# Kernel tuning notes

Measured on AMD Instinct MI355X. Metric: run time of the kernel, lower is better.

Reference implementation:

```python
import jax, jax.numpy as jnp
import numpy as np
import math

EMBED_DIM = 256
NUM_HEADS = 8
FFN_DIM = 1024
EPS = 1e-5


def layer_norm(x, g, b):
    mu = jnp.mean(x, axis=-1, keepdims=True)
    var = jnp.var(x, axis=-1, keepdims=True)
    return (x - mu) / jnp.sqrt(var + EPS) * g + b


def setup_inputs() -> dict:
    key = jax.random.key(0)
    ks = jax.random.split(key, 10)
    B, L, D, F = 4, 2048, EMBED_DIM, FFN_DIM
    x = jax.random.normal(ks[0], (B, L, D), dtype=jnp.float32)
    mask = jnp.ones((B, L), dtype=jnp.int32)
    # FFN params (PyTorch Linear default-ish scale)
    W1 = jax.random.normal(ks[1], (D, F), dtype=jnp.float32) / np.sqrt(D)
    b1 = jnp.zeros((F,), dtype=jnp.float32)
    W2 = jax.random.normal(ks[2], (F, D), dtype=jnp.float32) / np.sqrt(F)
    b2 = jnp.zeros((D,), dtype=jnp.float32)
    g1 = jnp.ones((D,), dtype=jnp.float32)
    be1 = jnp.zeros((D,), dtype=jnp.float32)
    g2 = jnp.ones((D,), dtype=jnp.float32)
    be2 = jnp.zeros((D,), dtype=jnp.float32)
    return {"x": x, "mask": mask, "W1": W1, "b1": b1, "W2": W2, "b2": b2,
            "g1": g1, "be1": be1, "g2": g2, "be2": be2}


def quantum_attention(x, mask):
    B, L, D = x.shape
    H, dk = NUM_HEADS, D // NUM_HEADS
    xh = x.reshape(B, L, H, dk).transpose(0, 2, 1, 3)  # [B,H,L,dk]
    # per-token mean over batch and heads -> [L, dk]
    m = jnp.mean(xh, axis=(0, 1))
    # closed form of the single-qubit RX circuit: P(|1>) = sin^2(angle/2)
    dot = m @ m.T  # [L, L]
    ang = jnp.clip(dot, -math.pi, math.pi)
    scores = jnp.sin(ang * 0.5) ** 2  # [L, L], shared across B and H
    attn = jnp.broadcast_to(scores[None, None], (B, H, L, L))
    attn = jnp.where(mask[:, None, None, :] == 0, -1e9, attn)
    attn = jax.nn.softmax(attn, axis=-1)
    out = jnp.einsum('bhij,bhjd->bhid', attn, xh)  # values are xh itself
    return out.transpose(0, 2, 1, 3).reshape(B, L, D)


def reference(x, mask, W1, b1, W2, b2, g1, be1, g2, be2):
    attn_out = quantum_attention(x, mask)
    h = layer_norm(x + attn_out, g1, be1)
    ffn = jax.nn.relu(h @ W1 + b1) @ W2 + b2
    return layer_norm(h + ffn, g2, be2)
```

## Files before the change

### kernel.cpp

```cpp
#include <hip/hip_runtime.h>
#include <hip/hip_bf16.h>


#define B_ 4
#define L_ 2048
#define D_ 256
#define F_ 1024
#define PI_F 3.14159265358979323846f

typedef __bf16 bf16x8 __attribute__((ext_vector_type(8)));
typedef float floatx4 __attribute__((ext_vector_type(4)));
typedef unsigned short ushortx4 __attribute__((ext_vector_type(4)));

#define WAIT_VM(n) asm volatile("s_waitcnt vmcnt(" #n ")" ::: "memory")
#define SCHED0() __builtin_amdgcn_sched_barrier(0)
#define BARRIER() do { SCHED0(); __builtin_amdgcn_s_barrier(); SCHED0(); } while (0)

__device__ __forceinline__ unsigned short f2bf(float f) {
    unsigned int u = __float_as_uint(f);
    u = (u + 0x7FFFu + ((u >> 16) & 1u)) >> 16;
    return (unsigned short)u;
}
__device__ __forceinline__ float bf2f(unsigned short u) {
    union { unsigned int i; float f; } v; v.i = ((unsigned int)u) << 16; return v.f;
}

__device__ __forceinline__ void async_cp16(unsigned short* lds, const unsigned short* g) {
    __builtin_amdgcn_global_load_lds(
        (const __attribute__((address_space(1))) unsigned int*)g,
        (__attribute__((address_space(3))) unsigned int*)lds, 16, 0, 0);
}

__global__ __launch_bounds__(256) void k_prep(const float* __restrict__ x,
                                              const float* __restrict__ W1,
                                              const float* __restrict__ W2,
                                              const int* __restrict__ mask,
                                              unsigned short* __restrict__ mb,
                                              unsigned short* __restrict__ XmT,
                                              unsigned short* __restrict__ W1T,
                                              unsigned short* __restrict__ W2T) {
    __shared__ float tile[32][33];
    int r = blockIdx.x, t = threadIdx.x;
    if (r >= 2560) {
        if (r < 2816) {
            int idx = (r - 2560) * 256 + t;
            int l = idx >> 5, k = idx & 31;
            float s = 0.f;
#pragma unroll
            for (int b = 0; b < B_; b++) {
                const float* xp = x + ((size_t)(b * L_ + l)) * D_ + k;
#pragma unroll
                for (int h = 0; h < 8; h++) s += xp[h * 32];
            }
            mb[idx] = f2bf(s * (1.f / 32.f));
        } else {
#pragma unroll
            for (int c = 0; c < 32; c++) {
                int e = c * 256 + t;
                int b = e >> 11, j = e & (L_ - 1);
                XmT[(size_t)(1024 + b) * L_ + j] = mask[b * L_ + j] ? 0x3F80 : 0;
            }
        }
        return;
    }
    const float* in; unsigned short* outp; int R, C; const int* mrow = nullptr; size_t bo = 0;
    int bx, by;
    if (r < 2048) {
        int z = r >> 9, rem = r & 511; by = rem >> 3; bx = rem & 7;
        in = x; outp = XmT; R = L_; C = 256; bo = (size_t)z * R * C; mrow = mask + z * L_;
    } else if (r < 2304) {
        int rem = r - 2048; bx = rem & 31; by = rem >> 5;
        in = W1; outp = W1T; R = 256; C = 1024;
    } else {
        int rem = r - 2304; bx = rem & 7; by = rem >> 3;
        in = W2; outp = W2T; R = 1024; C = 256;
    }
    int r0 = by * 32, c0 = bx * 32;
    int tx = t & 31, ty = t >> 5;
#pragma unroll
    for (int rr = 0; rr < 4; rr++) {
        int rw = ty + rr * 8;
        tile[rw][tx] = in[bo + (size_t)(r0 + rw) * C + c0 + tx];
    }
    float mfac = 1.f;
    if (mrow) mfac = mrow[r0 + tx] ? 1.f : 0.f;
    __syncthreads();
#pragma unroll
    for (int rr = 0; rr < 4; rr++) {
        int c = ty + rr * 8;
        outp[bo + (size_t)(c0 + c) * R + r0 + tx] = f2bf(tile[tx][c] * mfac);
    }
}

__global__ __launch_bounds__(256) void k_scores_mfma(const unsigned short* __restrict__ mb,
                                                     unsigned short* __restrict__ E) {
    const int t = threadIdx.x, lane = t & 63, wid = t >> 6;
    const int wm = (wid >> 1) * 64, wn = (wid & 1) * 32;
    const int lr = lane & 15, lq = lane >> 4;
    int m0 = blockIdx.y * 128, n0 = blockIdx.x * 64;
    bf16x8 af[4], bfr[2];
#pragma unroll
    for (int i = 0; i < 4; i++)
        af[i] = *(const bf16x8*)(mb + (size_t)(m0 + wm + i * 16 + lr) * 32 + lq * 8);
#pragma unroll
    for (int j = 0; j < 2; j++)
        bfr[j] = *(const bf16x8*)(mb + (size_t)(n0 + wn + j * 16 + lr) * 32 + lq * 8);
    floatx4 acc[4][2];
#pragma unroll
    for (int i = 0; i < 4; i++)
#pragma unroll
        for (int j = 0; j < 2; j++) {
            acc[i][j] = (floatx4){0.f, 0.f, 0.f, 0.f};
            acc[i][j] = __builtin_amdgcn_mfma_f32_16x16x32_bf16(af[i], bfr[j], acc[i][j], 0, 0, 0);
        }
#pragma unroll
    for (int i = 0; i < 4; i++)
#pragma unroll
        for (int j = 0; j < 2; j++)
#pragma unroll
            for (int r = 0; r < 4; r++) {
                int row = m0 + wm + i * 16 + lq * 4 + r;
                int col = n0 + wn + j * 16 + lr;
                float d = fminf(fmaxf(acc[i][j][r], -PI_F), PI_F);
                float sn = __sinf(0.5f * d);
                E[(size_t)row * L_ + col] = f2bf(__expf(sn * sn));
            }
}

__global__ __launch_bounds__(256) void k_av(const unsigned short* __restrict__ E,
                                            const unsigned short* __restrict__ XmT,
                                            unsigned short* __restrict__ Cb) {
    __shared__ __align__(16) unsigned short sbuf[3][128 * 64 + 64 * 64];
    const int t = threadIdx.x, lane = t & 63, wid = t >> 6;
    const int wm = (wid >> 1) * 64, wn = (wid & 1) * 32;
    const int lr = lane & 15, lq = lane >> 4;
    const int lrow = lane >> 3, lseg = lane & 7;

    int bid = blockIdx.x;
    int swz = (bid & 7) * 34 + (bid >> 3);
    int m0 = (swz / 17) * 128, n0 = (swz % 17) * 64;

    const unsigned short* Ag[4]; int sAoff[4];
#pragma unroll
    for (int q = 0; q < 4; q++) {
        int rl = wid * 32 + q * 8 + lrow;
        Ag[q] = E + (size_t)(m0 + rl) * L_ + ((lseg - rl) & 7) * 8;
        sAoff[q] = (wid * 32 + q * 8) * 64;
    }
    const unsigned short* Bg[2]; int sBoff[2];
#pragma unroll
    for (int q = 0; q < 2; q++) {
        int rl = wid * 16 + q * 8 + lrow;
        Bg[q] = XmT + (size_t)(n0 + rl) * L_ + ((lseg - rl) & 7) * 8;
        sBoff[q] = 8192 + (wid * 16 + q * 8) * 64;
    }
    int arot[4], aroff[4], brot[2], broff[2];
#pragma unroll
    for (int i = 0; i < 4; i++) { int ar = wm + i * 16 + lr; aroff[i] = ar * 64; arot[i] = lq + ar; }
#pragma unroll
    for (int j = 0; j < 2; j++) { int br = wn + j * 16 + lr; broff[j] = 8192 + br * 64; brot[j] = lq + br; }

    floatx4 acc[4][2];
#pragma unroll
    for (int i = 0; i < 4; i++)
#pragma unroll
        for (int j = 0; j < 2; j++) acc[i][j] = (floatx4){0.f, 0.f, 0.f, 0.f};

    auto stage = [&](unsigned short* base, int k0) {
#pragma unroll
        for (int q = 0; q < 4; q++) async_cp16(base + sAoff[q], Ag[q] + k0);
#pragma unroll
        for (int q = 0; q < 2; q++) async_cp16(base + sBoff[q], Bg[q] + k0);
    };
    auto compute = [&](const unsigned short* base) {
#pragma unroll
        for (int s = 0; s < 2; s++) {
            bf16x8 af[4], bfr[2];
#pragma unroll
            for (int i = 0; i < 4; i++)
                af[i] = *(const bf16x8*)(base + aroff[i] + ((s * 4 + arot[i]) & 7) * 8);
#pragma unroll
            for (int j = 0; j < 2; j++)
                bfr[j] = *(const bf16x8*)(base + broff[j] + ((s * 4 + brot[j]) & 7) * 8);
#pragma unroll
            for (int i = 0; i < 4; i++)
#pragma unroll
                for (int j = 0; j < 2; j++)
                    acc[i][j] = __builtin_amdgcn_mfma_f32_16x16x32_bf16(af[i], bfr[j], acc[i][j], 0, 0, 0);
        }
    };

    unsigned short *p0 = sbuf[0], *p1 = sbuf[1], *p2 = sbuf[2];
    stage(p0, 0); stage(p1, 64); stage(p2, 128);
    WAIT_VM(12); BARRIER();
    for (int p = 0; p < 29; ++p) {
        compute(p0);
        BARRIER();
        stage(p0, (p + 3) << 6);
        WAIT_VM(12); BARRIER();
        unsigned short* tmp = p0; p0 = p1; p1 = p2; p2 = tmp;
    }
    compute(p0);
    BARRIER();
    WAIT_VM(6); BARRIER();
    compute(p1);
    BARRIER();
    WAIT_VM(0); BARRIER();
    compute(p2);

#pragma unroll
    for (int i = 0; i < 4; i++)
#pragma unroll
        for (int j = 0; j < 2; j++)
#pragma unroll
            for (int r = 0; r < 4; r++) {
                int row = m0 + wm + i * 16 + lq * 4 + r;
                int col = n0 + wn + j * 16 + lr;
                Cb[(size_t)row * 1088 + col] = f2bf(acc[i][j][r]);
            }
}

__global__ __launch_bounds__(256) void k_ln1(const float* __restrict__ x, const unsigned short* __restrict__ Cb,
                                             const float* __restrict__ g_, const float* __restrict__ be_,
                                             unsigned short* __restrict__ hb) {
    int t = threadIdx.x, wid = t >> 6, lane = t & 63;
    int tok = (blockIdx.x << 2) + wid;
    int b = tok >> 11, i = tok & (L_ - 1);
    float rs = bf2f(Cb[(size_t)i * 1088 + 1024 + b]);
    float4 xv = *(const float4*)(x + (size_t)tok * D_ + lane * 4);
    ushortx4 cv = *(const ushortx4*)(Cb + (size_t)i * 1088 + b * 256 + lane * 4);
    float v0 = xv.x + bf2f(cv.x) / rs;
    float v1 = xv.y + bf2f(cv.y) / rs;
    float v2 = xv.z + bf2f(cv.z) / rs;
    float v3 = xv.w + bf2f(cv.w) / rs;
    float s  = v0 + v1 + v2 + v3;
    float s2 = v0 * v0 + v1 * v1 + v2 * v2 + v3 * v3;
#pragma unroll
    for (int o = 1; o < 64; o <<= 1) { s += __shfl_xor(s, o); s2 += __shfl_xor(s2, o); }
    float mu = s * (1.f / 256.f);
    float var = s2 * (1.f / 256.f) - mu * mu;
    float r = rsqrtf(var + 1e-5f);
    float4 gv = *(const float4*)(g_ + lane * 4);
    float4 bv = *(const float4*)(be_ + lane * 4);
    ushortx4 o4;
    o4.x = f2bf((v0 - mu) * r * gv.x + bv.x);
    o4.y = f2bf((v1 - mu) * r * gv.y + bv.y);
    o4.z = f2bf((v2 - mu) * r * gv.z + bv.z);
    o4.w = f2bf((v3 - mu) * r * gv.w + bv.w);
    *(ushortx4*)(hb + (size_t)tok * D_ + lane * 4) = o4;
}

__global__ __launch_bounds__(256) void k_gemm1(const unsigned short* __restrict__ hb,
                                               const unsigned short* __restrict__ W1T,
                                               const float* __restrict__ b1, unsigned short* __restrict__ t1) {
    __shared__ __align__(16) unsigned short sbuf[2][128 * 64 + 128 * 64];
    const int t = threadIdx.x, lane = t & 63, wid = t >> 6;
    const int wm = (wid >> 1) * 64, wn = (wid & 1) * 64;
    const int lr = lane & 15, lq = lane >> 4;
    const int lrow8 = lane >> 3, lseg = lane & 7;

    int bid = blockIdx.x;
    int swz = (bid & 7) * 64 + (bid >> 3);
    int m0 = (swz >> 3) * 128, n0 = (swz & 7) * 128;

    const unsigned short* Ag[4]; const unsigned short* Bg[4]; int aoff[4], boff4[4];
#pragma unroll
    for (int q = 0; q < 4; q++) {
        int rl = q * 32 + wid * 8 + lrow8;
        int seg = (lseg - rl) & 7;
        Ag[q] = hb + (size_t)(m0 + rl) * 256 + seg * 8;
        Bg[q] = W1T + (size_t)(n0 + rl) * 256 + seg * 8;
        aoff[q] = (q * 32 + wid * 8) * 64;
        boff4[q] = 8192 + (q * 32 + wid * 8) * 64;
    }
    int arot[4], aroff[4], brot[4], broff[4];
#pragma unroll
    for (int i = 0; i < 4; i++) { int ar = wm + i * 16 + lr; aroff[i] = ar * 64; arot[i] = lq + ar; }
#pragma unroll
    for (int j = 0; j < 4; j++) { int br = wn + j * 16 + lr; broff[j] = 8192 + br * 64; brot[j] = lq + br; }

    floatx4 acc[4][4];
#pragma unroll
    for (int i = 0; i < 4; i++)
#pragma unroll
        for (int j = 0; j < 4; j++) acc[i][j] = (floatx4){0.f, 0.f, 0.f, 0.f};

    auto stage = [&](unsigned short* base, int k0) {
#pragma unroll
        for (int q = 0; q < 4; q++) { async_cp16(base + aoff[q], Ag[q] + k0); async_cp16(base + boff4[q], Bg[q] + k0); }
    };
    auto compute = [&](const unsigned short* base) {
#pragma unroll
        for (int s = 0; s < 2; s++) {
            bf16x8 af[4], bfr[4];
#pragma unroll
            for (int i = 0; i < 4; i++) af[i] = *(const bf16x8*)(base + aroff[i] + ((s * 4 + arot[i]) & 7) * 8);
#pragma unroll
            for (int j = 0; j < 4; j++) bfr[j] = *(const bf16x8*)(base + broff[j] + ((s * 4 + brot[j]) & 7) * 8);
#pragma unroll
            for (int i = 0; i < 4; i++)
#pragma unroll
                for (int j = 0; j < 4; j++)
                    acc[i][j] = __builtin_amdgcn_mfma_f32_16x16x32_bf16(af[i], bfr[j], acc[i][j], 0, 0, 0);
        }
    };

    unsigned short *pa = sbuf[0], *pb = sbuf[1];
    stage(pa, 0); stage(pb, 64);
    WAIT_VM(8); BARRIER();
    compute(pa);
    BARRIER();
    stage(pa, 128);
    WAIT_VM(8); BARRIER();
    compute(pb);
    BARRIER();
    stage(pb, 192);
    WAIT_VM(8); BARRIER();
    compute(pa);
    BARRIER();
    WAIT_VM(0); BARRIER();
    compute(pb);

    float bb[4];
#pragma unroll
    for (int j = 0; j < 4; j++) bb[j] = b1[n0 + wn + j * 16 + lr];
#pragma unroll
    for (int i = 0; i < 4; i++)
#pragma unroll
        for (int j = 0; j < 4; j++) {
            int col = n0 + wn + j * 16 + lr;
#pragma unroll
            for (int r = 0; r < 4; r++) {
                int row = m0 + wm + i * 16 + lq * 4 + r;
                t1[(size_t)row * 1024 + col] = f2bf(fmaxf(acc[i][j][r] + bb[j], 0.f));
            }
        }
}

__global__ __launch_bounds__(256) void k_gemm2ln(const unsigned short* __restrict__ t1,
                                                 const unsigned short* __restrict__ W2T,
                                                 const float* __restrict__ b2,
                                                 const unsigned short* __restrict__ hb,
                                                 const float* __restrict__ g_, const float* __restrict__ be_,
                                                 float* __restrict__ out) {
    __shared__ __align__(16) unsigned short sbuf[3][32 * 64 + 256 * 64];
    __shared__ float red[2][32][2];
    const int t = threadIdx.x, lane = t & 63, wid = t >> 6;
    const int wm = (wid >> 1) * 16, wn = (wid & 1) * 128;
    const int lr = lane & 15, lq = lane >> 4;
    const int lrow8 = lane >> 3, lseg = lane & 7;
    int m0 = blockIdx.x * 32;

    int arl = wid * 8 + lrow8;
    const unsigned short* Ag = t1 + (size_t)(m0 + arl) * 1024 + (((lseg - arl) & 7) * 8);
    int sAoff = (wid * 8) * 64;
    const unsigned short* Bg[8]; int sBoff[8];
#pragma unroll
    for (int q = 0; q < 8; q++) {
        int rl = q * 32 + wid * 8 + lrow8;
        Bg[q] = W2T + (size_t)rl * 1024 + (((lseg - rl) & 7) * 8);
        sBoff[q] = 2048 + (q * 32 + wid * 8) * 64;
    }
    int aroff = (wm + lr) * 64, arot = lq + wm + lr;
    int brot[8], broff[8];
#pragma unroll
    for (int j = 0; j < 8; j++) { int br = wn + j * 16 + lr; broff[j] = 2048 + br * 64; brot[j] = lq + br; }

    floatx4 acc[8];
#pragma unroll
    for (int j = 0; j < 8; j++) acc[j] = (floatx4){0.f, 0.f, 0.f, 0.f};

    auto stage = [&](unsigned short* base, int k0) {
        async_cp16(base + sAoff, Ag + k0);
#pragma unroll
        for (int q = 0; q < 8; q++) async_cp16(base + sBoff[q], Bg[q] + k0);
    };
    auto compute = [&](const unsigned short* base) {
#pragma unroll
        for (int s = 0; s < 2; s++) {
            bf16x8 af = *(const bf16x8*)(base + aroff + ((s * 4 + arot) & 7) * 8);
#pragma unroll
            for (int j = 0; j < 8; j++) {
                bf16x8 bfr = *(const bf16x8*)(base + broff[j] + ((s * 4 + brot[j]) & 7) * 8);
                acc[j] = __builtin_amdgcn_mfma_f32_16x16x32_bf16(af, bfr, acc[j], 0, 0, 0);
            }
        }
    };

    unsigned short *p0 = sbuf[0], *p1 = sbuf[1], *p2 = sbuf[2];
    stage(p0, 0); stage(p1, 64); stage(p2, 128);
    WAIT_VM(18); BARRIER();
    for (int p = 0; p < 13; ++p) {
        compute(p0);
        BARRIER();
        stage(p0, (p + 3) << 6);
        WAIT_VM(18); BARRIER();
        unsigned short* tmp = p0; p0 = p1; p1 = p2; p2 = tmp;
    }
    compute(p0);
    BARRIER();
    WAIT_VM(9); BARRIER();
    compute(p1);
    BARRIER();
    WAIT_VM(0); BARRIER();
    compute(p2);

    float psum[4], psq[4];
#pragma unroll
    for (int r = 0; r < 4; r++) { psum[r] = 0.f; psq[r] = 0.f; }
#pragma unroll
    for (int j = 0; j < 8; j++) {
        int col = wn + j * 16 + lr;
        float bv = b2[col];
#pragma unroll
        for (int r = 0; r < 4; r++) {
            int row = m0 + wm + lq * 4 + r;
            float v = acc[j][r] + bv + bf2f(hb[(size_t)row * 256 + col]);
            acc[j][r] = v;
            psum[r] += v; psq[r] += v * v;
        }
    }
#pragma unroll
    for (int o = 1; o < 16; o <<= 1) {
#pragma unroll
        for (int r = 0; r < 4; r++) { psum[r] += __shfl_xor(psum[r], o); psq[r] += __shfl_xor(psq[r], o); }
    }
    if (lr == 0) {
#pragma unroll
        for (int r = 0; r < 4; r++) {
            int lrow = wm + lq * 4 + r;
            red[wid & 1][lrow][0] = psum[r];
            red[wid & 1][lrow][1] = psq[r];
        }
    }
    __syncthreads();
#pragma unroll
    for (int r = 0; r < 4; r++) {
        int lrow = wm + lq * 4 + r;
        float s = red[0][lrow][0] + red[1][lrow][0];
        float s2 = red[0][lrow][1] + red[1][lrow][1];
        float mu = s * (1.f / 256.f);
        float var = s2 * (1.f / 256.f) - mu * mu;
        float rc = rsqrtf(var + 1e-5f);
        int row = m0 + lrow;
#pragma unroll
        for (int j = 0; j < 8; j++) {
            int col = wn + j * 16 + lr;
            out[(size_t)row * 256 + col] = (acc[j][r] - mu) * rc * g_[col] + be_[col];
        }
    }
}

extern "C" void kernel_launch(void* const* d_in, const int* in_sizes, int n_in,
                              void* d_out, int out_size, void* d_ws, size_t ws_size,
                              hipStream_t stream) {
    const float* x   = (const float*)d_in[0];
    const int*  mask = (const int*)d_in[1];
    const float* W1  = (const float*)d_in[2];
    const float* b1  = (const float*)d_in[3];
    const float* W2  = (const float*)d_in[4];
    const float* b2  = (const float*)d_in[5];
    const float* g1  = (const float*)d_in[6];
    const float* be1 = (const float*)d_in[7];
    const float* g2  = (const float*)d_in[8];
    const float* be2 = (const float*)d_in[9];
    float* out = (float*)d_out;

    char* w = (char*)d_ws;
    unsigned short* mb_   = (unsigned short*)w;  w += 65536 * 2;
    unsigned short* E_    = (unsigned short*)w;  w += (size_t)L_ * L_ * 2;
    unsigned short* XmT_  = (unsigned short*)w;  w += (size_t)1088 * L_ * 2;
    unsigned short* W1T_  = (unsigned short*)w;  w += 262144 * 2;
    unsigned short* W2T_  = (unsigned short*)w;  w += 262144 * 2;
    unsigned short* Cb_   = (unsigned short*)w;  w += (size_t)L_ * 1088 * 2;
    unsigned short* hb_   = (unsigned short*)w;  w += (size_t)8192 * 256 * 2;
    unsigned short* t1_   = (unsigned short*)w;  w += (size_t)8192 * 1024 * 2;

    k_prep<<<2817, 256, 0, stream>>>(x, W1, W2, mask, mb_, XmT_, W1T_, W2T_);
    k_scores_mfma<<<dim3(32, 16), 256, 0, stream>>>(mb_, E_);
    k_av<<<272, 256, 0, stream>>>(E_, XmT_, Cb_);
    k_ln1<<<2048, 256, 0, stream>>>(x, Cb_, g1, be1, hb_);
    k_gemm1<<<512, 256, 0, stream>>>(hb_, W1T_, b1, t1_);
    k_gemm2ln<<<256, 256, 0, stream>>>(t1_, W2T_, b2, hb_, g2, be2, out);
}
```

Measured before the change: 139.9 us.

## Compute softmax row sums in scores kernel and retile gemm2ln warps

The masked softmax denominators were previously produced by extra mask columns in the AV GEMM (1088 wide). They are now computed as per-block partial row sums inside the scores kernel and reduced in the LN1 kernel. This shrinks the AV GEMM to 1024 columns (256 blocks instead of 272), which removes a partial wave and drops the mask-column setup in prep. The gemm2ln kernel is also retiled so each warp covers 32x64 instead of 16x128, sharing B fragments across two A rows, at the cost of a 4-way LDS reduction.

```diff
diff --git a/kernel.cpp b/kernel.cpp
--- a/kernel.cpp
+++ b/kernel.cpp
@@ -42,25 +42,16 @@
     __shared__ float tile[32][33];
     int r = blockIdx.x, t = threadIdx.x;
     if (r >= 2560) {
-        if (r < 2816) {
-            int idx = (r - 2560) * 256 + t;
-            int l = idx >> 5, k = idx & 31;
-            float s = 0.f;
-#pragma unroll
-            for (int b = 0; b < B_; b++) {
-                const float* xp = x + ((size_t)(b * L_ + l)) * D_ + k;
-#pragma unroll
-                for (int h = 0; h < 8; h++) s += xp[h * 32];
-            }
-            mb[idx] = f2bf(s * (1.f / 32.f));
-        } else {
-#pragma unroll
-            for (int c = 0; c < 32; c++) {
-                int e = c * 256 + t;
-                int b = e >> 11, j = e & (L_ - 1);
-                XmT[(size_t)(1024 + b) * L_ + j] = mask[b * L_ + j] ? 0x3F80 : 0;
-            }
-        }
+        int idx = (r - 2560) * 256 + t;
+        int l = idx >> 5, k = idx & 31;
+        float s = 0.f;
+#pragma unroll
+        for (int b = 0; b < B_; b++) {
+            const float* xp = x + ((size_t)(b * L_ + l)) * D_ + k;
+#pragma unroll
+            for (int h = 0; h < 8; h++) s += xp[h * 32];
+        }
+        mb[idx] = f2bf(s * (1.f / 32.f));
         return;
     }
     const float* in; unsigned short* outp; int R, C; const int* mrow = nullptr; size_t bo = 0;
@@ -93,7 +84,10 @@
 }
 
 __global__ __launch_bounds__(256) void k_scores_mfma(const unsigned short* __restrict__ mb,
-                                                     unsigned short* __restrict__ E) {
+                                                     const int* __restrict__ mask,
+                                                     unsigned short* __restrict__ E,
+                                                     float* __restrict__ rowpart) {
+    __shared__ float part[128][2][4];
     const int t = threadIdx.x, lane = t & 63, wid = t >> 6;
     const int wm = (wid >> 1) * 64, wn = (wid & 1) * 32;
     const int lr = lane & 15, lq = lane >> 4;
@@ -113,8 +107,14 @@
             acc[i][j] = (floatx4){0.f, 0.f, 0.f, 0.f};
             acc[i][j] = __builtin_amdgcn_mfma_f32_16x16x32_bf16(af[i], bfr[j], acc[i][j], 0, 0, 0);
         }
-#pragma unroll
-    for (int i = 0; i < 4; i++)
+    float mv[4][2];
+#pragma unroll
+    for (int b = 0; b < 4; b++) {
+        mv[b][0] = mask[b * L_ + n0 + wn + lr] ? 1.f : 0.f;
+        mv[b][1] = mask[b * L_ + n0 + wn + 16 + lr] ? 1.f : 0.f;
+    }
+#pragma unroll
+    for (int i = 0; i < 4; i++) {
 #pragma unroll
         for (int j = 0; j < 2; j++)
 #pragma unroll
@@ -123,8 +123,34 @@
                 int col = n0 + wn + j * 16 + lr;
                 float d = fminf(fmaxf(acc[i][j][r], -PI_F), PI_F);
                 float sn = __sinf(0.5f * d);
-                E[(size_t)row * L_ + col] = f2bf(__expf(sn * sn));
-            }
+                float e = __expf(sn * sn);
+                acc[i][j][r] = e;
+                E[(size_t)row * L_ + col] = f2bf(e);
+            }
+#pragma unroll
+        for (int r = 0; r < 4; r++) {
+            float pb[4];
+#pragma unroll
+            for (int b = 0; b < 4; b++)
+                pb[b] = acc[i][0][r] * mv[b][0] + acc[i][1][r] * mv[b][1];
+#pragma unroll
+            for (int o = 1; o < 16; o <<= 1)
+#pragma unroll
+                for (int b = 0; b < 4; b++) pb[b] += __shfl_xor(pb[b], o);
+            if (lr == 0) {
+                int lrow = wm + i * 16 + lq * 4 + r;
+#pragma unroll
+                for (int b = 0; b < 4; b++) part[lrow][wid & 1][b] = pb[b];
+            }
+        }
+    }
+    __syncthreads();
+    if (t < 128) {
+        int grow = m0 + t;
+#pragma unroll
+        for (int b = 0; b < 4; b++)
+            rowpart[((size_t)grow * 4 + b) * 32 + blockIdx.x] = part[t][0][b] + part[t][1][b];
+    }
 }
 
 __global__ __launch_bounds__(256) void k_av(const unsigned short* __restrict__ E,
@@ -137,8 +163,8 @@
     const int lrow = lane >> 3, lseg = lane & 7;
 
     int bid = blockIdx.x;
-    int swz = (bid & 7) * 34 + (bid >> 3);
-    int m0 = (swz / 17) * 128, n0 = (swz % 17) * 64;
+    int swz = (bid & 7) * 32 + (bid >> 3);
+    int m0 = (swz >> 4) * 128, n0 = (swz & 15) * 64;
 
     const unsigned short* Ag[4]; int sAoff[4];
 #pragma unroll
@@ -216,19 +242,23 @@
             for (int r = 0; r < 4; r++) {
                 int row = m0 + wm + i * 16 + lq * 4 + r;
                 int col = n0 + wn + j * 16 + lr;
-                Cb[(size_t)row * 1088 + col] = f2bf(acc[i][j][r]);
+                Cb[(size_t)row * 1024 + col] = f2bf(acc[i][j][r]);
             }
 }
 
 __global__ __launch_bounds__(256) void k_ln1(const float* __restrict__ x, const unsigned short* __restrict__ Cb,
+                                             const float* __restrict__ rowpart,
                                              const float* __restrict__ g_, const float* __restrict__ be_,
                                              unsigned short* __restrict__ hb) {
     int t = threadIdx.x, wid = t >> 6, lane = t & 63;
     int tok = (blockIdx.x << 2) + wid;
     int b = tok >> 11, i = tok & (L_ - 1);
-    float rs = bf2f(Cb[(size_t)i * 1088 + 1024 + b]);
+    float rp = rowpart[((size_t)i * 4 + b) * 32 + (lane & 31)];
+#pragma unroll
+    for (int o = 1; o < 32; o <<= 1) rp += __shfl_xor(rp, o);
+    float rs = rp;
     float4 xv = *(const float4*)(x + (size_t)tok * D_ + lane * 4);
-    ushortx4 cv = *(const ushortx4*)(Cb + (size_t)i * 1088 + b * 256 + lane * 4);
+    ushortx4 cv = *(const ushortx4*)(Cb + (size_t)i * 1024 + b * 256 + lane * 4);
     float v0 = xv.x + bf2f(cv.x) / rs;
     float v1 = xv.y + bf2f(cv.y) / rs;
     float v2 = xv.z + bf2f(cv.z) / rs;
@@ -344,9 +374,9 @@
                                                  const float* __restrict__ g_, const float* __restrict__ be_,
                                                  float* __restrict__ out) {
     __shared__ __align__(16) unsigned short sbuf[3][32 * 64 + 256 * 64];
-    __shared__ float red[2][32][2];
+    __shared__ float red[4][32][2];
     const int t = threadIdx.x, lane = t & 63, wid = t >> 6;
-    const int wm = (wid >> 1) * 16, wn = (wid & 1) * 128;
+    const int wn = wid * 64;
     const int lr = lane & 15, lq = lane >> 4;
     const int lrow8 = lane >> 3, lseg = lane & 7;
     int m0 = blockIdx.x * 32;
@@ -361,14 +391,18 @@
         Bg[q] = W2T + (size_t)rl * 1024 + (((lseg - rl) & 7) * 8);
         sBoff[q] = 2048 + (q * 32 + wid * 8) * 64;
     }
-    int aroff = (wm + lr) * 64, arot = lq + wm + lr;
-    int brot[8], broff[8];
-#pragma unroll
-    for (int j = 0; j < 8; j++) { int br = wn + j * 16 + lr; broff[j] = 2048 + br * 64; brot[j] = lq + br; }
-
-    floatx4 acc[8];
-#pragma unroll
-    for (int j = 0; j < 8; j++) acc[j] = (floatx4){0.f, 0.f, 0.f, 0.f};
+    int aroff[2], arot[2];
+#pragma unroll
+    for (int i = 0; i < 2; i++) { int ar = i * 16 + lr; aroff[i] = ar * 64; arot[i] = lq + ar; }
+    int brot[4], broff[4];
+#pragma unroll
+    for (int j = 0; j < 4; j++) { int br = wn + j * 16 + lr; broff[j] = 2048 + br * 64; brot[j] = lq + br; }
+
+    floatx4 acc[2][4];
+#pragma unroll
+    for (int i = 0; i < 2; i++)
+#pragma unroll
+        for (int j = 0; j < 4; j++) acc[i][j] = (floatx4){0.f, 0.f, 0.f, 0.f};
 
     auto stage = [&](unsigned short* base, int k0) {
         async_cp16(base + sAoff, Ag + k0);
@@ -378,11 +412,16 @@
     auto compute = [&](const unsigned short* base) {
 #pragma unroll
         for (int s = 0; s < 2; s++) {
-            bf16x8 af = *(const bf16x8*)(base + aroff + ((s * 4 + arot) & 7) * 8);
-#pragma unroll
-            for (int j = 0; j < 8; j++) {
+            bf16x8 af[2];
+#pragma unroll
+            for (int i = 0; i < 2; i++)
+                af[i] = *(const bf16x8*)(base + aroff[i] + ((s * 4 + arot[i]) & 7) * 8);
+#pragma unroll
+            for (int j = 0; j < 4; j++) {
                 bf16x8 bfr = *(const bf16x8*)(base + broff[j] + ((s * 4 + brot[j]) & 7) * 8);
-                acc[j] = __builtin_amdgcn_mfma_f32_16x16x32_bf16(af, bfr, acc[j], 0, 0, 0);
+#pragma unroll
+                for (int i = 0; i < 2; i++)
+                    acc[i][j] = __builtin_amdgcn_mfma_f32_16x16x32_bf16(af[i], bfr, acc[i][j], 0, 0, 0);
             }
         }
     };
@@ -405,50 +444,59 @@
     WAIT_VM(0); BARRIER();
     compute(p2);
 
-    float psum[4], psq[4];
-#pragma unroll
-    for (int r = 0; r < 4; r++) { psum[r] = 0.f; psq[r] = 0.f; }
-#pragma unroll
-    for (int j = 0; j < 8; j++) {
-        int col = wn + j * 16 + lr;
-        float bv = b2[col];
+    float psum[2][4], psq[2][4];
+#pragma unroll
+    for (int i = 0; i < 2; i++)
+#pragma unroll
+        for (int r = 0; r < 4; r++) { psum[i][r] = 0.f; psq[i][r] = 0.f; }
+#pragma unroll
+    for (int i = 0; i < 2; i++)
+#pragma unroll
+        for (int j = 0; j < 4; j++) {
+            int col = wn + j * 16 + lr;
+            float bv = b2[col];
+#pragma unroll
+            for (int r = 0; r < 4; r++) {
+                int row = m0 + i * 16 + lq * 4 + r;
+                float v = acc[i][j][r] + bv + bf2f(hb[(size_t)row * 256 + col]);
+                acc[i][j][r] = v;
+                psum[i][r] += v; psq[i][r] += v * v;
+            }
+        }
+#pragma unroll
+    for (int o = 1; o < 16; o <<= 1)
+#pragma unroll
+        for (int i = 0; i < 2; i++)
+#pragma unroll
+            for (int r = 0; r < 4; r++) { psum[i][r] += __shfl_xor(psum[i][r], o); psq[i][r] += __shfl_xor(psq[i][r], o); }
+    if (lr == 0) {
+#pragma unroll
+        for (int i = 0; i < 2; i++)
+#pragma unroll
+            for (int r = 0; r < 4; r++) {
+                int lrow = i * 16 + lq * 4 + r;
+                red[wid][lrow][0] = psum[i][r];
+                red[wid][lrow][1] = psq[i][r];
+            }
+    }
+    __syncthreads();
+#pragma unroll
+    for (int i = 0; i < 2; i++)
 #pragma unroll
         for (int r = 0; r < 4; r++) {
-            int row = m0 + wm + lq * 4 + r;
-            float v = acc[j][r] + bv + bf2f(hb[(size_t)row * 256 + col]);
-            acc[j][r] = v;
-            psum[r] += v; psq[r] += v * v;
-        }
-    }
-#pragma unroll
-    for (int o = 1; o < 16; o <<= 1) {
-#pragma unroll
-        for (int r = 0; r < 4; r++) { psum[r] += __shfl_xor(psum[r], o); psq[r] += __shfl_xor(psq[r], o); }
-    }
-    if (lr == 0) {
-#pragma unroll
-        for (int r = 0; r < 4; r++) {
-            int lrow = wm + lq * 4 + r;
-            red[wid & 1][lrow][0] = psum[r];
-            red[wid & 1][lrow][1] = psq[r];
-        }
-    }
-    __syncthreads();
-#pragma unroll
-    for (int r = 0; r < 4; r++) {
-        int lrow = wm + lq * 4 + r;
-        float s = red[0][lrow][0] + red[1][lrow][0];
-        float s2 = red[0][lrow][1] + red[1][lrow][1];
-        float mu = s * (1.f / 256.f);
-        float var = s2 * (1.f / 256.f) - mu * mu;
-        float rc = rsqrtf(var + 1e-5f);
-        int row = m0 + lrow;
-#pragma unroll
-        for (int j = 0; j < 8; j++) {
-            int col = wn + j * 16 + lr;
-            out[(size_t)row * 256 + col] = (acc[j][r] - mu) * rc * g_[col] + be_[col];
-        }
-    }
+            int lrow = i * 16 + lq * 4 + r;
+            float s  = red[0][lrow][0] + red[1][lrow][0] + red[2][lrow][0] + red[3][lrow][0];
+            float s2 = red[0][lrow][1] + red[1][lrow][1] + red[2][lrow][1] + red[3][lrow][1];
+            float mu = s * (1.f / 256.f);
+            float var = s2 * (1.f / 256.f) - mu * mu;
+            float rc = rsqrtf(var + 1e-5f);
+            int row = m0 + lrow;
+#pragma unroll
+            for (int j = 0; j < 4; j++) {
+                int col = wn + j * 16 + lr;
+                out[(size_t)row * 256 + col] = (acc[i][j][r] - mu) * rc * g_[col] + be_[col];
+            }
+        }
 }
 
 extern "C" void kernel_launch(void* const* d_in, const int* in_sizes, int n_in,
@@ -469,17 +517,18 @@
     char* w = (char*)d_ws;
     unsigned short* mb_   = (unsigned short*)w;  w += 65536 * 2;
     unsigned short* E_    = (unsigned short*)w;  w += (size_t)L_ * L_ * 2;
-    unsigned short* XmT_  = (unsigned short*)w;  w += (size_t)1088 * L_ * 2;
+    unsigned short* XmT_  = (unsigned short*)w;  w += (size_t)1024 * L_ * 2;
     unsigned short* W1T_  = (unsigned short*)w;  w += 262144 * 2;
     unsigned short* W2T_  = (unsigned short*)w;  w += 262144 * 2;
-    unsigned short* Cb_   = (unsigned short*)w;  w += (size_t)L_ * 1088 * 2;
+    unsigned short* Cb_   = (unsigned short*)w;  w += (size_t)L_ * 1024 * 2;
     unsigned short* hb_   = (unsigned short*)w;  w += (size_t)8192 * 256 * 2;
     unsigned short* t1_   = (unsigned short*)w;  w += (size_t)8192 * 1024 * 2;
-
-    k_prep<<<2817, 256, 0, stream>>>(x, W1, W2, mask, mb_, XmT_, W1T_, W2T_);
-    k_scores_mfma<<<dim3(32, 16), 256, 0, stream>>>(mb_, E_);
-    k_av<<<272, 256, 0, stream>>>(E_, XmT_, Cb_);
-    k_ln1<<<2048, 256, 0, stream>>>(x, Cb_, g1, be1, hb_);
+    float*          rp_   = (float*)w;           w += (size_t)2048 * 4 * 32 * 4;
+
+    k_prep<<<2816, 256, 0, stream>>>(x, W1, W2, mask, mb_, XmT_, W1T_, W2T_);
+    k_scores_mfma<<<dim3(32, 16), 256, 0, stream>>>(mb_, mask, E_, rp_);
+    k_av<<<256, 256, 0, stream>>>(E_, XmT_, Cb_);
+    k_ln1<<<2048, 256, 0, stream>>>(x, Cb_, rp_, g1, be1, hb_);
     k_gemm1<<<512, 256, 0, stream>>>(hb_, W1T_, b1, t1_);
     k_gemm2ln<<<256, 256, 0, stream>>>(t1_, W2T_, b2, hb_, g2, be2, out);
 }
```

Result: slower. 143.2 us (+2.4%).
